# Performance work log

Measured on AMD Instinct MI355X. Metric: run time of the kernel, lower is better.

The kernel has to match this reference:

```python
import jax, jax.numpy as jnp
from jax import lax
import numpy as np

# ---- geometry constants (from metadata / module __init__) ----
NA = 1152            # rotview (number of projection angles)
ND = 736             # det_count
NP = 512             # reconstructed image size
VOX = 1.0 / 0.7      # vox_scaling
D   = VOX * 595.0    # source-to-isocenter distance
DD  = VOX * 490.6    # isocenter-to-detector distance
DU  = VOX * 1.2858   # detector pixel spacing
DSD = D + DD         # source-to-detector distance
ANGLES = np.linspace(0.0, 2.0 * np.pi, NA, endpoint=False) + np.pi / 2.0

# ---- Shepp-Logan Fourier filter (skimage/torch-radon construction) ----
PAD = max(64, int(2 ** np.ceil(np.log2(2 * ND))))  # 2048

def _shepp_logan_filter(size):
    n = np.concatenate([np.arange(1, size // 2 + 1, 2),
                        np.arange(size // 2 - 1, 0, -2)])
    f = np.zeros(size)
    f[0] = 0.25
    f[1::2] = -1.0 / (np.pi * n) ** 2
    four = 2.0 * np.real(np.fft.fft(f))            # ramp filter
    omega = np.pi * np.fft.fftfreq(size)[1:]
    four[1:] *= np.sin(omega) / omega              # Shepp-Logan window
    return four[: size // 2 + 1].astype(np.float32)  # rfft half-spectrum

FILT = jnp.asarray(_shepp_logan_filter(PAD))
COS_A = jnp.asarray(np.cos(ANGLES).astype(np.float32))
SIN_A = jnp.asarray(np.sin(ANGLES).astype(np.float32))


def _filter_sinogram(sino):
    # sino: (NA, ND). Zero-pad to PAD, filter in Fourier domain, crop.
    padded = jnp.pad(sino, ((0, 0), (0, PAD - ND)))
    spec = jnp.fft.rfft(padded, axis=-1) * FILT
    filt = jnp.fft.irfft(spec, n=PAD, axis=-1)[:, :ND]
    return filt * (np.pi / (2.0 * NA))


def _backproject(filtered):
    # Pixel-driven fan-beam (flat detector) backprojection.
    c = (NP - 1) / 2.0
    coords = jnp.arange(NP, dtype=jnp.float32) - c
    ys, xs = jnp.meshgrid(coords, coords, indexing='ij')  # (NP, NP)

    def body(acc, inp):
        cb, sb, row = inp
        pdot = xs * cb + ys * sb            # pixel coord along source dir
        pe = -xs * sb + ys * cb             # pixel coord along detector axis
        den = D - pdot                      # source->pixel depth
        u = DSD * pe / den                  # detector coordinate (mm)
        iu = u / DU + (ND - 1) / 2.0        # fractional detector index
        i0 = jnp.floor(iu)
        frac = iu - i0
        i0i = i0.astype(jnp.int32)
        valid = (i0i >= 0) & (i0i < ND - 1) & (den > 0)
        i0c = jnp.clip(i0i, 0, ND - 2)
        v = row[i0c] * (1.0 - frac) + row[i0c + 1] * frac  # linear interp
        w = (D / den) ** 2                   # fan-beam distance weighting
        return acc + jnp.where(valid, w * v, 0.0), None

    img, _ = lax.scan(body, jnp.zeros((NP, NP), jnp.float32),
                      (COS_A, SIN_A, filtered))
    return img


def setup_inputs() -> dict:
    key = jax.random.key(0)
    x = jax.random.normal(key, (1, 1, NA, ND), dtype=jnp.float32)
    return {"x": x}


def reference(x):
    sino = x[0, 0]                          # (NA, ND) after squeeze
    filtered = _filter_sinogram(sino)
    fbp = _backproject(filtered)
    # mu -> HU -> normalize to [0, 1] window
    fbp_hu = (1000.0 * ((fbp - 0.0192) / 0.0192) - (-1024.0)) / (3072.0 - (-1024.0))
    return fbp_hu[None, None]               # (1, 1, 512, 512)
```

## Files before the change

kernel.cpp:

```cpp
#include <hip/hip_runtime.h>
#include <math.h>

#ifndef M_PI
#define M_PI 3.14159265358979323846
#endif

#define NAANG 1152
#define NDET  736
#define NPIX  512
#define PADN  2048
#define NHALF 1025

#define OFF_FILTF 0
#define OFF_H     4224
#define OFF_TRIG  12416
#define OFF_FS    30848
#define OFF_PART  3422336

typedef float f32x2 __attribute__((ext_vector_type(2)));

static __device__ __forceinline__ f32x2 load2(const float* p) {
    f32x2 r;
    __builtin_memcpy(&r, p, 8);
    return r;
}

__global__ void filt_spec_kernel(float* __restrict__ filt_f) {
    __shared__ float red[256];
    const int m = blockIdx.x;
    const int t = threadIdx.x;
    float s = 0.f;
    for (int j = t; j < 1024; j += 256) {
        int n = (j < 512) ? (2 * j + 1) : (2047 - 2 * j);
        float fj = (float)(-1.0 / ((M_PI * n) * (M_PI * n)));
        int r = (m * (2 * j + 1)) & (PADN - 1);
        s += fj * cospif((float)r * (1.0f / 1024.0f));
    }
    red[t] = s;
    __syncthreads();
    for (int w = 128; w > 0; w >>= 1) {
        if (t < w) red[t] += red[t + w];
        __syncthreads();
    }
    if (t == 0) {
        double four = 2.0 * (0.25 + (double)red[0]);
        if (m > 0) {
            double om = M_PI * (double)m / (double)PADN;
            four *= sin(om) / om;
        }
        filt_f[m] = (float)four;
    }
}

__global__ void h_kernel(const float* __restrict__ filt_f,
                         float* __restrict__ h, float4* __restrict__ trig) {
    __shared__ float red[256];
    const int k = blockIdx.x;
    const int t = threadIdx.x;
    if (t == 0 && k < NAANG) {
        double ang = 2.0 * M_PI * (double)k / (double)NAANG + M_PI / 2.0;
        double c = cos(ang), s = sin(ang);
        double K = 1085.6 / 1.2858;
        trig[k] = make_float4((float)c, (float)s, (float)(K * c), (float)(K * s));
    }
    float s = 0.f;
    for (int m = t; m <= 1024; m += 256) {
        float F = filt_f[m];
        float c;
        if (m == 0) c = 1.f;
        else if (m == 1024) c = (k & 1) ? -1.f : 1.f;
        else c = 2.f * cospif((float)((m * k) & (PADN - 1)) * (1.0f / 1024.0f));
        s += F * c;
    }
    red[t] = s;
    __syncthreads();
    for (int w = 128; w > 0; w >>= 1) {
        if (t < w) red[t] += red[t + w];
        __syncthreads();
    }
    if (t == 0)
        h[k] = (float)((double)red[0] / (double)PADN * (M_PI / (2.0 * (double)NAANG)));
}

__global__ void conv_kernel(const float* __restrict__ x,
                            const float* __restrict__ h,
                            float* __restrict__ fs) {
    __shared__ float sh2[2816];
    __shared__ float srow[2][NDET];
    const int t = threadIdx.x;
    const int row0 = blockIdx.x * 2;
    const float4* h4 = (const float4*)h;
    for (int i = t; i < 704; i += 192) ((float4*)sh2)[i] = h4[i & 511];
    const float4* x4 = (const float4*)(x + (size_t)row0 * NDET);
    for (int i = t; i < 368; i += 192) ((float4*)srow[0])[i] = x4[i];
    __syncthreads();

    const int r = t / 96;
    const int u = t % 96;
    const float* my = srow[r];
    const int A0 = 8 * u + PADN;
    float o[8] = {0.f, 0.f, 0.f, 0.f, 0.f, 0.f, 0.f, 0.f};
    #pragma unroll 2
    for (int j = 0; j < NDET; j += 8) {
        float4 s0 = *(const float4*)&my[j];
        float4 s1 = *(const float4*)&my[j + 4];
        const float* hp = &sh2[A0 - j - 8];
        float4 h0 = *(const float4*)(hp);
        float4 h1 = *(const float4*)(hp + 4);
        float4 h2 = *(const float4*)(hp + 8);
        float4 h3 = *(const float4*)(hp + 12);
        float wv[16] = {h0.x, h0.y, h0.z, h0.w, h1.x, h1.y, h1.z, h1.w,
                        h2.x, h2.y, h2.z, h2.w, h3.x, h3.y, h3.z, h3.w};
        float se[8]  = {s0.x, s0.y, s0.z, s0.w, s1.x, s1.y, s1.z, s1.w};
        #pragma unroll
        for (int e = 0; e < 8; ++e) {
            #pragma unroll
            for (int d = 0; d < 8; ++d)
                o[d] = fmaf(se[e], wv[8 + d - e], o[d]);
        }
    }
    if (u < 92) {
        float* op = fs + (size_t)(row0 + r) * NDET + 8 * u;
        *(float4*)op       = make_float4(o[0], o[1], o[2], o[3]);
        *(float4*)(op + 4) = make_float4(o[4], o[5], o[6], o[7]);
    }
}

#define GEO(AA, QQ, G0,G1,G2,G3, FR0,FR1,FR2,FR3, W0,W1,W2,W3)           \
  {                                                                      \
    const float* rp = fs + (size_t)(abase + (AA)) * NDET;                \
    float den0 = fmaf(-xs, QQ.x, fmaf(-ys0, QQ.y, Dg));                  \
    float kpe0 = fmaf(ys0, QQ.z, -(xs * QQ.w));                          \
    float sb2 = QQ.y + QQ.y, kc2 = QQ.z + QQ.z;                          \
    float den1 = den0 - QQ.y, den2 = den0 - sb2, den3 = den2 - QQ.y;     \
    float kpe1 = kpe0 + QQ.z, kpe2 = kpe0 + kc2, kpe3 = kpe2 + QQ.z;     \
    float r0 = __builtin_amdgcn_rcpf(den0);                              \
    float r1 = __builtin_amdgcn_rcpf(den1);                              \
    float r2 = __builtin_amdgcn_rcpf(den2);                              \
    float r3 = __builtin_amdgcn_rcpf(den3);                              \
    float iu0 = fmaf(kpe0, r0, 367.5f);                                  \
    float iu1 = fmaf(kpe1, r1, 367.5f);                                  \
    float iu2 = fmaf(kpe2, r2, 367.5f);                                  \
    float iu3 = fmaf(kpe3, r3, 367.5f);                                  \
    float f0 = floorf(iu0), f1 = floorf(iu1);                            \
    float f2 = floorf(iu2), f3 = floorf(iu3);                            \
    int i0 = (int)f0, i1 = (int)f1, i2 = (int)f2, i3 = (int)f3;          \
    int c0 = min(max(i0, 0), NDET - 2);                                  \
    int c1 = min(max(i1, 0), NDET - 2);                                  \
    int c2 = min(max(i2, 0), NDET - 2);                                  \
    int c3 = min(max(i3, 0), NDET - 2);                                  \
    G0 = load2(rp + c0); G1 = load2(rp + c1);                            \
    G2 = load2(rp + c2); G3 = load2(rp + c3);                            \
    FR0 = iu0 - f0; FR1 = iu1 - f1; FR2 = iu2 - f2; FR3 = iu3 - f3;      \
    W0 = ((unsigned)i0 < (unsigned)(NDET - 1)) ? r0 * r0 : 0.f;          \
    W1 = ((unsigned)i1 < (unsigned)(NDET - 1)) ? r1 * r1 : 0.f;          \
    W2 = ((unsigned)i2 < (unsigned)(NDET - 1)) ? r2 * r2 : 0.f;          \
    W3 = ((unsigned)i3 < (unsigned)(NDET - 1)) ? r3 * r3 : 0.f;          \
  }

#define CONSUME(G0,G1,G2,G3, FR0,FR1,FR2,FR3, W0,W1,W2,W3)               \
  {                                                                      \
    float v0 = fmaf(FR0, G0.y - G0.x, G0.x);                             \
    float v1 = fmaf(FR1, G1.y - G1.x, G1.x);                             \
    float v2 = fmaf(FR2, G2.y - G2.x, G2.x);                             \
    float v3 = fmaf(FR3, G3.y - G3.x, G3.x);                             \
    acc0 = fmaf(W0, v0, acc0); acc1 = fmaf(W1, v1, acc1);                \
    acc2 = fmaf(W2, v2, acc2); acc3 = fmaf(W3, v3, acc3);                \
  }

template<int NCH>
__global__ __launch_bounds__(256, 8)
void backproj_kernel(const float* __restrict__ fs,
                     const float4* __restrict__ trig,
                     float* __restrict__ partial) {
    constexpr int ACL = NAANG / NCH;
    const int t = threadIdx.x;
    const int lane = t & 63, wave = t >> 6;
    const int lx = lane & 15, lq = lane >> 4;
    const int wx = wave & 1,  wy = wave >> 1;
    const int X = blockIdx.x * 32 + wx * 16 + lx;
    const int Y = blockIdx.y * 32 + wy * 16 + lq * 4;
    const int abase = blockIdx.z * ACL;
    const float xs  = (float)X - 255.5f;
    const float ys0 = (float)Y - 255.5f;
    const float Dg = 850.0f;

    float acc0 = 0.f, acc1 = 0.f, acc2 = 0.f, acc3 = 0.f;
    f32x2 Ag0, Ag1, Ag2, Ag3, Bg0, Bg1, Bg2, Bg3;
    float Af0, Af1, Af2, Af3, Aw0, Aw1, Aw2, Aw3;
    float Bf0, Bf1, Bf2, Bf3, Bw0, Bw1, Bw2, Bw3;

    float4 qc = trig[abase];
    float4 qn = trig[abase + 1];
    GEO(0, qc, Ag0,Ag1,Ag2,Ag3, Af0,Af1,Af2,Af3, Aw0,Aw1,Aw2,Aw3);
    int a = 0;
    for (; a + 2 < ACL; a += 2) {
        float4 q2 = trig[abase + a + 2];
        GEO(a + 1, qn, Bg0,Bg1,Bg2,Bg3, Bf0,Bf1,Bf2,Bf3, Bw0,Bw1,Bw2,Bw3);
        CONSUME(Ag0,Ag1,Ag2,Ag3, Af0,Af1,Af2,Af3, Aw0,Aw1,Aw2,Aw3);
        qn = trig[abase + a + 3];
        GEO(a + 2, q2, Ag0,Ag1,Ag2,Ag3, Af0,Af1,Af2,Af3, Aw0,Aw1,Aw2,Aw3);
        CONSUME(Bg0,Bg1,Bg2,Bg3, Bf0,Bf1,Bf2,Bf3, Bw0,Bw1,Bw2,Bw3);
    }
    GEO(ACL - 1, qn, Bg0,Bg1,Bg2,Bg3, Bf0,Bf1,Bf2,Bf3, Bw0,Bw1,Bw2,Bw3);
    CONSUME(Ag0,Ag1,Ag2,Ag3, Af0,Af1,Af2,Af3, Aw0,Aw1,Aw2,Aw3);
    CONSUME(Bg0,Bg1,Bg2,Bg3, Bf0,Bf1,Bf2,Bf3, Bw0,Bw1,Bw2,Bw3);

    float* outp = partial + ((size_t)blockIdx.z * NPIX + Y) * NPIX + X;
    outp[0 * NPIX] = acc0;
    outp[1 * NPIX] = acc1;
    outp[2 * NPIX] = acc2;
    outp[3 * NPIX] = acc3;
}

template<int NCH>
__global__ void combine_kernel(const float* __restrict__ partial,
                               float* __restrict__ out) {
    int p = blockIdx.x * 256 + threadIdx.x;
    float s = 0.f;
    #pragma unroll
    for (int c = 0; c < NCH; ++c) s += partial[c * NPIX * NPIX + p];
    const float scale = (float)(722500.0 * 1000.0 / 0.0192 / 4096.0);
    out[p] = fmaf(s, scale, 0.005859375f);
}

extern "C" void kernel_launch(void* const* d_in, const int* in_sizes, int n_in,
                              void* d_out, int out_size, void* d_ws, size_t ws_size,
                              hipStream_t stream) {
    const float* x = (const float*)d_in[0];
    float* out = (float*)d_out;

    char* ws = (char*)d_ws;
    float*  filt_f = (float*)(ws + OFF_FILTF);
    float*  h      = (float*)(ws + OFF_H);
    float4* trig   = (float4*)(ws + OFF_TRIG);
    float*  fs     = (float*)(ws + OFF_FS);
    float*  part   = (float*)(ws + OFF_PART);

    filt_spec_kernel<<<NHALF, 256, 0, stream>>>(filt_f);
    h_kernel<<<PADN, 256, 0, stream>>>(filt_f, h, trig);
    conv_kernel<<<NAANG / 2, 192, 0, stream>>>(x, h, fs);

    const size_t pbytes = (size_t)NPIX * NPIX * 4;
    if (ws_size >= OFF_PART + 8 * pbytes) {
        backproj_kernel<8><<<dim3(16, 16, 8), 256, 0, stream>>>(fs, trig, part);
        combine_kernel<8><<<NPIX * NPIX / 256, 256, 0, stream>>>(part, out);
    } else if (ws_size >= OFF_PART + 4 * pbytes) {
        backproj_kernel<4><<<dim3(16, 16, 4), 256, 0, stream>>>(fs, trig, part);
        combine_kernel<4><<<NPIX * NPIX / 256, 256, 0, stream>>>(part, out);
    } else if (ws_size >= OFF_PART + 2 * pbytes) {
        backproj_kernel<2><<<dim3(16, 16, 2), 256, 0, stream>>>(fs, trig, part);
        combine_kernel<2><<<NPIX * NPIX / 256, 256, 0, stream>>>(part, out);
    } else {
        backproj_kernel<1><<<dim3(16, 16, 1), 256, 0, stream>>>(fs, trig, part);
        combine_kernel<1><<<NPIX * NPIX / 256, 256, 0, stream>>>(part, out);
    }
}
```

Baseline: 269.4 us.

## Store filtered sinogram as packed fp16 neighbor pairs for backprojection gathers

The convolution kernel now writes each filtered detector sample as a half2 holding the value and its right neighbour, staging results in shared memory to fetch the neighbour. The backprojection then gathers one 4-byte half2 per pixel-angle instead of an 8-byte unaligned float pair, and converts to float before interpolating. This halves the gather traffic and cache footprint of the sinogram and aligns the loads, at the cost of fp16 rounding of the filtered data, which may hurt accuracy.

Measured after the change: 279.8 us. +3.9%, slower.

```diff
diff --git a/kernel.cpp b/kernel.cpp
--- a/kernel.cpp
+++ b/kernel.cpp
@@ -1,4 +1,5 @@
 #include <hip/hip_runtime.h>
+#include <hip/hip_fp16.h>
 #include <math.h>
 
 #ifndef M_PI
@@ -16,14 +17,6 @@
 #define OFF_TRIG  12416
 #define OFF_FS    30848
 #define OFF_PART  3422336
-
-typedef float f32x2 __attribute__((ext_vector_type(2)));
-
-static __device__ __forceinline__ f32x2 load2(const float* p) {
-    f32x2 r;
-    __builtin_memcpy(&r, p, 8);
-    return r;
-}
 
 __global__ void filt_spec_kernel(float* __restrict__ filt_f) {
     __shared__ float red[256];
@@ -84,7 +77,7 @@
 
 __global__ void conv_kernel(const float* __restrict__ x,
                             const float* __restrict__ h,
-                            float* __restrict__ fs) {
+                            __half2* __restrict__ fsh) {
     __shared__ float sh2[2816];
     __shared__ float srow[2][NDET];
     const int t = threadIdx.x;
@@ -119,16 +112,28 @@
                 o[d] = fmaf(se[e], wv[8 + d - e], o[d]);
         }
     }
+    __syncthreads();
     if (u < 92) {
-        float* op = fs + (size_t)(row0 + r) * NDET + 8 * u;
-        *(float4*)op       = make_float4(o[0], o[1], o[2], o[3]);
-        *(float4*)(op + 4) = make_float4(o[4], o[5], o[6], o[7]);
+        #pragma unroll
+        for (int d = 0; d < 8; ++d) srow[r][8 * u + d] = o[d];
+    }
+    __syncthreads();
+    if (u < 92) {
+        float nb = (u < 91) ? srow[r][8 * u + 8] : 0.f;
+        __half2 pk[8];
+        #pragma unroll
+        for (int d = 0; d < 7; ++d)
+            pk[d] = __floats2half2_rn(o[d], o[d + 1]);
+        pk[7] = __floats2half2_rn(o[7], nb);
+        __half2* op = fsh + (size_t)(row0 + r) * NDET + 8 * u;
+        *(float4*)op       = *(float4*)&pk[0];
+        *(float4*)(op + 4) = *(float4*)&pk[4];
     }
 }
 
 #define GEO(AA, QQ, G0,G1,G2,G3, FR0,FR1,FR2,FR3, W0,W1,W2,W3)           \
   {                                                                      \
-    const float* rp = fs + (size_t)(abase + (AA)) * NDET;                \
+    const __half2* rp = fsh + (size_t)(abase + (AA)) * NDET;             \
     float den0 = fmaf(-xs, QQ.x, fmaf(-ys0, QQ.y, Dg));                  \
     float kpe0 = fmaf(ys0, QQ.z, -(xs * QQ.w));                          \
     float sb2 = QQ.y + QQ.y, kc2 = QQ.z + QQ.z;                          \
@@ -149,8 +154,7 @@
     int c1 = min(max(i1, 0), NDET - 2);                                  \
     int c2 = min(max(i2, 0), NDET - 2);                                  \
     int c3 = min(max(i3, 0), NDET - 2);                                  \
-    G0 = load2(rp + c0); G1 = load2(rp + c1);                            \
-    G2 = load2(rp + c2); G3 = load2(rp + c3);                            \
+    G0 = rp[c0]; G1 = rp[c1]; G2 = rp[c2]; G3 = rp[c3];                  \
     FR0 = iu0 - f0; FR1 = iu1 - f1; FR2 = iu2 - f2; FR3 = iu3 - f3;      \
     W0 = ((unsigned)i0 < (unsigned)(NDET - 1)) ? r0 * r0 : 0.f;          \
     W1 = ((unsigned)i1 < (unsigned)(NDET - 1)) ? r1 * r1 : 0.f;          \
@@ -160,17 +164,21 @@
 
 #define CONSUME(G0,G1,G2,G3, FR0,FR1,FR2,FR3, W0,W1,W2,W3)               \
   {                                                                      \
-    float v0 = fmaf(FR0, G0.y - G0.x, G0.x);                             \
-    float v1 = fmaf(FR1, G1.y - G1.x, G1.x);                             \
-    float v2 = fmaf(FR2, G2.y - G2.x, G2.x);                             \
-    float v3 = fmaf(FR3, G3.y - G3.x, G3.x);                             \
+    float2 F0 = __half22float2(G0);                                      \
+    float2 F1 = __half22float2(G1);                                      \
+    float2 F2 = __half22float2(G2);                                      \
+    float2 F3 = __half22float2(G3);                                      \
+    float v0 = fmaf(FR0, F0.y - F0.x, F0.x);                             \
+    float v1 = fmaf(FR1, F1.y - F1.x, F1.x);                             \
+    float v2 = fmaf(FR2, F2.y - F2.x, F2.x);                             \
+    float v3 = fmaf(FR3, F3.y - F3.x, F3.x);                             \
     acc0 = fmaf(W0, v0, acc0); acc1 = fmaf(W1, v1, acc1);                \
     acc2 = fmaf(W2, v2, acc2); acc3 = fmaf(W3, v3, acc3);                \
   }
 
 template<int NCH>
 __global__ __launch_bounds__(256, 8)
-void backproj_kernel(const float* __restrict__ fs,
+void backproj_kernel(const __half2* __restrict__ fsh,
                      const float4* __restrict__ trig,
                      float* __restrict__ partial) {
     constexpr int ACL = NAANG / NCH;
@@ -186,7 +194,7 @@
     const float Dg = 850.0f;
 
     float acc0 = 0.f, acc1 = 0.f, acc2 = 0.f, acc3 = 0.f;
-    f32x2 Ag0, Ag1, Ag2, Ag3, Bg0, Bg1, Bg2, Bg3;
+    __half2 Ag0, Ag1, Ag2, Ag3, Bg0, Bg1, Bg2, Bg3;
     float Af0, Af1, Af2, Af3, Aw0, Aw1, Aw2, Aw3;
     float Bf0, Bf1, Bf2, Bf3, Bw0, Bw1, Bw2, Bw3;
 
@@ -231,28 +239,28 @@
     float* out = (float*)d_out;
 
     char* ws = (char*)d_ws;
-    float*  filt_f = (float*)(ws + OFF_FILTF);
-    float*  h      = (float*)(ws + OFF_H);
-    float4* trig   = (float4*)(ws + OFF_TRIG);
-    float*  fs     = (float*)(ws + OFF_FS);
-    float*  part   = (float*)(ws + OFF_PART);
+    float*   filt_f = (float*)(ws + OFF_FILTF);
+    float*   h      = (float*)(ws + OFF_H);
+    float4*  trig   = (float4*)(ws + OFF_TRIG);
+    __half2* fsh    = (__half2*)(ws + OFF_FS);
+    float*   part   = (float*)(ws + OFF_PART);
 
     filt_spec_kernel<<<NHALF, 256, 0, stream>>>(filt_f);
     h_kernel<<<PADN, 256, 0, stream>>>(filt_f, h, trig);
-    conv_kernel<<<NAANG / 2, 192, 0, stream>>>(x, h, fs);
+    conv_kernel<<<NAANG / 2, 192, 0, stream>>>(x, h, fsh);
 
     const size_t pbytes = (size_t)NPIX * NPIX * 4;
     if (ws_size >= OFF_PART + 8 * pbytes) {
-        backproj_kernel<8><<<dim3(16, 16, 8), 256, 0, stream>>>(fs, trig, part);
+        backproj_kernel<8><<<dim3(16, 16, 8), 256, 0, stream>>>(fsh, trig, part);
         combine_kernel<8><<<NPIX * NPIX / 256, 256, 0, stream>>>(part, out);
     } else if (ws_size >= OFF_PART + 4 * pbytes) {
-        backproj_kernel<4><<<dim3(16, 16, 4), 256, 0, stream>>>(fs, trig, part);
+        backproj_kernel<4><<<dim3(16, 16, 4), 256, 0, stream>>>(fsh, trig, part);
         combine_kernel<4><<<NPIX * NPIX / 256, 256, 0, stream>>>(part, out);
     } else if (ws_size >= OFF_PART + 2 * pbytes) {
-        backproj_kernel<2><<<dim3(16, 16, 2), 256, 0, stream>>>(fs, trig, part);
+        backproj_kernel<2><<<dim3(16, 16, 2), 256, 0, stream>>>(fsh, trig, part);
         combine_kernel<2><<<NPIX * NPIX / 256, 256, 0, stream>>>(part, out);
     } else {
-        backproj_kernel<1><<<dim3(16, 16, 1), 256, 0, stream>>>(fs, trig, part);
+        backproj_kernel<1><<<dim3(16, 16, 1), 256, 0, stream>>>(fsh, trig, part);
         combine_kernel<1><<<NPIX * NPIX / 256, 256, 0, stream>>>(part, out);
     }
 }
```
